# Kernel tuning notes

Hardware: AMD Instinct MI355X
Metric: run time of the kernel (lower is better)

Reference implementation:

```python
import jax, jax.numpy as jnp
import numpy as np

HEADS = 8
DIM_HEAD = 64


def setup_inputs() -> dict:
    key = jax.random.key(0)
    ks = jax.random.split(key, 4)
    B, C, H, W = 1, 256, 64, 64
    inner = HEADS * DIM_HEAD  # 512
    x = jax.random.normal(ks[0], (B, C, H, W), dtype=jnp.float32)
    norm_w = jnp.ones((C,), dtype=jnp.float32)                      # RMSNorm weight (1,C,1,1) flattened
    w_qkv = jax.random.normal(ks[1], (3 * inner, C), dtype=jnp.float32) * 0.02  # 1x1 conv, no bias
    w_out = jax.random.normal(ks[2], (C, inner), dtype=jnp.float32) * 0.02      # 1x1 conv
    b_out = jax.random.normal(ks[3], (C,), dtype=jnp.float32) * 0.02
    return {"x": x, "norm_w": norm_w, "w_qkv": w_qkv, "w_out": w_out, "b_out": b_out}


def reference(x, norm_w, w_qkv, w_out, b_out):
    B, C, H, W = x.shape
    N = H * W
    # RMSNorm: F.normalize over channel dim (L2, eps clamp) * weight * sqrt(C)
    l2 = jnp.sqrt(jnp.sum(x * x, axis=1, keepdims=True))
    xn = x / jnp.maximum(l2, 1e-12) * norm_w[None, :, None, None] * (C ** 0.5)
    # 1x1 conv QKV = channel matmul
    qkv = jnp.einsum('oc,bchw->bohw', w_qkv, xn)  # [B, 3*inner, H, W]
    q, k, v = jnp.split(qkv, 3, axis=1)

    def split_heads(t):
        # 'b (h d) x y -> b h (x y) d'
        return t.reshape(B, HEADS, DIM_HEAD, N).transpose(0, 1, 3, 2)

    q, k, v = map(split_heads, (q, k, v))
    scale = DIM_HEAD ** -0.5
    scores = jnp.einsum('bhnd,bhmd->bhnm', q, k) * scale  # [B,H,N,N]
    attn = jax.nn.softmax(scores, axis=-1)
    out = jnp.einsum('bhnm,bhmd->bhnd', attn, v)
    # 'b h (x y) d -> b (h d) x y'
    out = out.transpose(0, 1, 3, 2).reshape(B, HEADS * DIM_HEAD, H, W)
    # output 1x1 conv + residual (note: residual is the NORMALIZED x, per source)
    return jnp.einsum('ci,bihw->bchw', w_out, out) + b_out[None, :, None, None] + xn
```

## Files before the change

kernel.cpp:

```cpp
#include <hip/hip_runtime.h>


#define NPIX 4096
#define CIN 256
#define INNER 512
#define NHEAD 8
#define DH 64

typedef _Float16 f16;
typedef __attribute__((ext_vector_type(8))) _Float16 f16x8;
typedef __attribute__((ext_vector_type(4))) float f32x4;

static __device__ __forceinline__ f32x4 mfma_f16(f16x8 a, f16x8 b, f32x4 c) {
  return __builtin_amdgcn_mfma_f32_16x16x32_f16(a, b, c, 0, 0, 0);
}

static __device__ __forceinline__ unsigned pk2(float lo, float hi) {
  return __builtin_bit_cast(unsigned, __builtin_amdgcn_cvt_pkrtz(lo, hi));
}

__global__ __launch_bounds__(256) void k_cvt(const float* __restrict__ a,
                                             f16* __restrict__ b, int n) {
  int i = blockIdx.x * 256 + threadIdx.x;
  if (i < n) b[i] = (f16)a[i];
}

__global__ __launch_bounds__(256) void k_rmsnorm(const float* __restrict__ x,
                                                 const float* __restrict__ w,
                                                 float* __restrict__ xn,
                                                 f16* __restrict__ xnT) {
  const int pi = threadIdx.x & 15, cs = threadIdx.x >> 4;
  const int p = blockIdx.x * 16 + pi;
  __shared__ float red[16][16];
  float ss = 0.f;
  for (int i = 0; i < 16; ++i) {
    float v = x[(cs * 16 + i) * NPIX + p];
    ss += v * v;
  }
  red[cs][pi] = ss;
  __syncthreads();
  float tot = 0.f;
#pragma unroll
  for (int s = 0; s < 16; ++s) tot += red[s][pi];
  float inv = 16.0f / fmaxf(sqrtf(tot), 1e-12f);
  for (int i = 0; i < 16; ++i) {
    int c = cs * 16 + i;
    float v = x[c * NPIX + p] * inv * w[c];
    xn[c * NPIX + p] = v;
    xnT[p * CIN + c] = (f16)v;
  }
}

__global__ __launch_bounds__(256) void k_qkv(const f16* __restrict__ wqkv,
                                             const f16* __restrict__ xnT,
                                             f16* __restrict__ qT,
                                             f16* __restrict__ kT,
                                             f16* __restrict__ vv) {
  const int lane = threadIdx.x & 63, wave = threadIdx.x >> 6;
  const int l15 = lane & 15, quad = lane >> 4;
  const int obase = blockIdx.y * 64 + (wave >> 1) * 32;
  const int pbase = blockIdx.x * 128 + (wave & 1) * 64;
  const int sect = blockIdx.y >> 3;
  f32x4 acc[8];
#pragma unroll
  for (int i = 0; i < 8; ++i) acc[i] = (f32x4){0.f, 0.f, 0.f, 0.f};
#pragma unroll
  for (int kc = 0; kc < CIN / 32; ++kc) {
    f16x8 af[2], bfr[4];
#pragma unroll
    for (int oc = 0; oc < 2; ++oc)
      af[oc] = *(const f16x8*)(wqkv + (size_t)(obase + oc * 16 + l15) * CIN + kc * 32 + quad * 8);
#pragma unroll
    for (int pc = 0; pc < 4; ++pc)
      bfr[pc] = *(const f16x8*)(xnT + (size_t)(pbase + pc * 16 + l15) * CIN + kc * 32 + quad * 8);
    if (sect < 2) {
#pragma unroll
      for (int pc = 0; pc < 4; ++pc)
#pragma unroll
        for (int oc = 0; oc < 2; ++oc)
          acc[pc * 2 + oc] = mfma_f16(bfr[pc], af[oc], acc[pc * 2 + oc]);
    } else {
#pragma unroll
      for (int oc = 0; oc < 2; ++oc)
#pragma unroll
        for (int pc = 0; pc < 4; ++pc)
          acc[oc * 4 + pc] = mfma_f16(af[oc], bfr[pc], acc[oc * 4 + pc]);
    }
  }
  if (sect < 2) {
    f16* dst = (sect == 0) ? qT : kT;
    const float sc = (sect == 0) ? 0.18033688f : 1.0f;
    const int head = blockIdx.y & 7;
    const int dd = (wave >> 1) * 32;
#pragma unroll
    for (int pc = 0; pc < 4; ++pc)
#pragma unroll
      for (int oc = 0; oc < 2; ++oc)
#pragma unroll
        for (int r = 0; r < 4; ++r) {
          int p = pbase + pc * 16 + quad * 4 + r;
          dst[((size_t)(head << 12) + p) * DH + dd + oc * 16 + l15] =
              (f16)(acc[pc * 2 + oc][r] * sc);
        }
  } else {
#pragma unroll
    for (int oc = 0; oc < 2; ++oc)
#pragma unroll
      for (int r = 0; r < 4; ++r) {
        int o = obase + oc * 16 + quad * 4 + r - 2 * INNER;
#pragma unroll
        for (int pc = 0; pc < 4; ++pc)
          vv[(size_t)o * NPIX + pbase + pc * 16 + l15] = (f16)acc[oc * 4 + pc][r];
      }
  }
}

__global__ __launch_bounds__(256, 2) void k_attn(const f16* __restrict__ qT,
                                                 const f16* __restrict__ kT,
                                                 const f16* __restrict__ vv,
                                                 f16* __restrict__ Ows) {
  const int head = blockIdx.y;
  const int tid = threadIdx.x;
  const int wave = tid >> 6, lane = tid & 63;
  const int l15 = lane & 15, quad = lane >> 4;
  const int qb = blockIdx.x * 64;

  __shared__ float Om[4][4][64][17];
  __shared__ float Ll[4][4][16];

  f16x8 qf[4][2];
#pragma unroll
  for (int qt = 0; qt < 4; ++qt)
#pragma unroll
    for (int kc = 0; kc < 2; ++kc)
      qf[qt][kc] = *(const f16x8*)(qT + ((size_t)(head << 12) + qb + qt * 16 + l15) * DH + kc * 32 + quad * 8);

  f32x4 o[4][4], ol[4];
#pragma unroll
  for (int qt = 0; qt < 4; ++qt) {
#pragma unroll
    for (int c = 0; c < 4; ++c) o[qt][c] = (f32x4){0.f, 0.f, 0.f, 0.f};
    ol[qt] = (f32x4){0.f, 0.f, 0.f, 0.f};
  }

  const f16* kbase = kT + (size_t)(head << 12) * DH;
  const f16* vbase = vv + (size_t)(head * DH) * NPIX;
  const int kb0 = wave * (NPIX / 4);
  const int srcA = ((quad & 1) << 5) + l15;
  const int srcB = srcA + 16;
  const bool hiQuad = quad >= 2;
  const f16x8 onesv = {1.f16, 1.f16, 1.f16, 1.f16, 1.f16, 1.f16, 1.f16, 1.f16};

  f16x8 kf[2][2], kfn[2][2];
#pragma unroll
  for (int nc = 0; nc < 2; ++nc)
#pragma unroll
    for (int kc = 0; kc < 2; ++kc)
      kf[nc][kc] = *(const f16x8*)(kbase + (size_t)(kb0 + nc * 16 + l15) * DH + kc * 32 + quad * 8);

  for (int it = 0; it < 32; ++it) {
    const int kb = kb0 + it * 32;
    f16x8 vf[4];
#pragma unroll
    for (int c = 0; c < 4; ++c)
      vf[c] = *(const f16x8*)(vbase + (size_t)(c * 16 + l15) * NPIX + kb + quad * 8);
    const int kbn = kb0 + ((it + 1) & 31) * 32;
#pragma unroll
    for (int nc = 0; nc < 2; ++nc)
#pragma unroll
      for (int kc = 0; kc < 2; ++kc)
        kfn[nc][kc] = *(const f16x8*)(kbase + (size_t)(kbn + nc * 16 + l15) * DH + kc * 32 + quad * 8);

    f32x4 s[4][2];
#pragma unroll
    for (int qt = 0; qt < 4; ++qt)
#pragma unroll
      for (int nc = 0; nc < 2; ++nc) {
        s[qt][nc] = mfma_f16(kf[nc][0], qf[qt][0], (f32x4){0.f, 0.f, 0.f, 0.f});
        s[qt][nc] = mfma_f16(kf[nc][1], qf[qt][1], s[qt][nc]);
      }

#pragma unroll
    for (int qt = 0; qt < 4; ++qt) {
      float p0[4], p1[4];
#pragma unroll
      for (int r = 0; r < 4; ++r) {
        p0[r] = __builtin_amdgcn_exp2f(s[qt][0][r]);
        p1[r] = __builtin_amdgcn_exp2f(s[qt][1][r]);
      }
      unsigned A0 = pk2(p0[0], p0[1]), B0 = pk2(p0[2], p0[3]);
      unsigned A1 = pk2(p1[0], p1[1]), B1 = pk2(p1[2], p1[3]);
      unsigned As = hiQuad ? A1 : A0;
      unsigned Bs = hiQuad ? B1 : B0;
      union { f16x8 v; unsigned u[4]; } pf;
      pf.u[0] = (unsigned)__shfl((int)As, srcA);
      pf.u[1] = (unsigned)__shfl((int)Bs, srcA);
      pf.u[2] = (unsigned)__shfl((int)As, srcB);
      pf.u[3] = (unsigned)__shfl((int)Bs, srcB);
#pragma unroll
      for (int c = 0; c < 4; ++c) o[qt][c] = mfma_f16(vf[c], pf.v, o[qt][c]);
      ol[qt] = mfma_f16(onesv, pf.v, ol[qt]);
    }

#pragma unroll
    for (int nc = 0; nc < 2; ++nc)
#pragma unroll
      for (int kc = 0; kc < 2; ++kc) kf[nc][kc] = kfn[nc][kc];
  }

#pragma unroll
  for (int qt = 0; qt < 4; ++qt) {
    if (quad == 0) Ll[wave][qt][l15] = ol[qt][0];
#pragma unroll
    for (int c = 0; c < 4; ++c)
#pragma unroll
      for (int r = 0; r < 4; ++r)
        Om[wave][qt][c * 16 + quad * 4 + r][l15] = o[qt][c][r];
  }
  __syncthreads();

  const int d = tid & 63;
  const int qg = tid >> 6;
#pragma unroll
  for (int qt = 0; qt < 4; ++qt)
#pragma unroll
    for (int i = 0; i < 4; ++i) {
      int q = qg * 4 + i;
      float O = Om[0][qt][d][q] + Om[1][qt][d][q] + Om[2][qt][d][q] + Om[3][qt][d][q];
      float L = Ll[0][qt][q] + Ll[1][qt][q] + Ll[2][qt][q] + Ll[3][qt][q];
      Ows[((size_t)(head << 12) + qb + qt * 16 + q) * DH + d] = (f16)(O / L);
    }
}

__global__ __launch_bounds__(256) void k_oproj(const f16* __restrict__ wout,
                                               const f16* __restrict__ Ows,
                                               const float* __restrict__ bout,
                                               const float* __restrict__ xn,
                                               float* __restrict__ out) {
  const int lane = threadIdx.x & 63, wave = threadIdx.x >> 6;
  const int l15 = lane & 15, quad = lane >> 4;
  const int mbase = blockIdx.y * 32 + (wave >> 1) * 16;
  const int pbase = blockIdx.x * 64 + (wave & 1) * 32;
  f32x4 acc[2];
  acc[0] = (f32x4){0.f, 0.f, 0.f, 0.f};
  acc[1] = (f32x4){0.f, 0.f, 0.f, 0.f};
#pragma unroll
  for (int kc = 0; kc < INNER / 32; ++kc) {
    f16x8 af = *(const f16x8*)(wout + (size_t)(mbase + l15) * INNER + kc * 32 + quad * 8);
    int i0 = kc * 32 + quad * 8;
    int head = i0 >> 6, d0 = i0 & 63;
#pragma unroll
    for (int pc = 0; pc < 2; ++pc) {
      f16x8 bfr = *(const f16x8*)(Ows + ((size_t)(head << 12) + pbase + pc * 16 + l15) * DH + d0);
      acc[pc] = mfma_f16(af, bfr, acc[pc]);
    }
  }
#pragma unroll
  for (int pc = 0; pc < 2; ++pc)
#pragma unroll
    for (int r = 0; r < 4; ++r) {
      int c = mbase + quad * 4 + r, p = pbase + pc * 16 + l15;
      out[c * NPIX + p] = acc[pc][r] + bout[c] + xn[c * NPIX + p];
    }
}

extern "C" void kernel_launch(void* const* d_in, const int* in_sizes, int n_in,
                              void* d_out, int out_size, void* d_ws, size_t ws_size,
                              hipStream_t stream) {
  (void)in_sizes; (void)n_in; (void)out_size; (void)ws_size;
  const float* x      = (const float*)d_in[0];
  const float* norm_w = (const float*)d_in[1];
  const float* w_qkv  = (const float*)d_in[2];
  const float* w_out  = (const float*)d_in[3];
  const float* b_out  = (const float*)d_in[4];
  float* out = (float*)d_out;

  char* ws = (char*)d_ws;
  float* xn    = (float*)(ws);
  f16* xnT     = (f16*)(ws + (4u << 20));
  f16* qT      = (f16*)(ws + (6u << 20));
  f16* kT      = (f16*)(ws + (10u << 20));
  f16* vv      = (f16*)(ws + (14u << 20));
  f16* Ows     = (f16*)(ws + (18u << 20));
  f16* wqkv_h  = (f16*)(ws + (22u << 20));
  f16* wout_h  = (f16*)(ws + (23u << 20));

  hipLaunchKernelGGL(k_cvt, dim3((3 * INNER * CIN + 255) / 256), dim3(256), 0, stream,
                     w_qkv, wqkv_h, 3 * INNER * CIN);
  hipLaunchKernelGGL(k_cvt, dim3((CIN * INNER + 255) / 256), dim3(256), 0, stream,
                     w_out, wout_h, CIN * INNER);
  hipLaunchKernelGGL(k_rmsnorm, dim3(NPIX / 16), dim3(256), 0, stream, x, norm_w, xn, xnT);
  hipLaunchKernelGGL(k_qkv, dim3(NPIX / 128, 1536 / 64), dim3(256), 0, stream,
                     wqkv_h, xnT, qT, kT, vv);
  hipLaunchKernelGGL(k_attn, dim3(NPIX / 64, NHEAD), dim3(256), 0, stream,
                     qT, kT, vv, Ows);
  hipLaunchKernelGGL(k_oproj, dim3(NPIX / 64, CIN / 32), dim3(256), 0, stream,
                     wout_h, Ows, b_out, xn, out);
}
```

Before: 168.4 us.

## Pack attention partials to fp16 in LDS, raise occupancy, fuse weight conversions

The two fp32-to-fp16 weight conversion kernels are merged into one launch that converts two elements per thread. The attention kernel stores per-wave partial outputs in shared memory as packed fp16 pairs instead of fp32, roughly halving LDS usage, and raises the occupancy hint from 2 to 4 blocks. The grid is flattened with the head in the low bits so neighbouring blocks work on different heads. The final reduction writes packed fp16 pairs and multiplies by a reciprocal instead of dividing. Rounding the partial sums to fp16 before the cross-wave reduction slightly reduces precision, and the higher occupancy target may cause register spills.

```diff
diff --git a/kernel.cpp b/kernel.cpp
--- a/kernel.cpp
+++ b/kernel.cpp
@@ -19,10 +19,28 @@
   return __builtin_bit_cast(unsigned, __builtin_amdgcn_cvt_pkrtz(lo, hi));
 }
 
-__global__ __launch_bounds__(256) void k_cvt(const float* __restrict__ a,
-                                             f16* __restrict__ b, int n) {
-  int i = blockIdx.x * 256 + threadIdx.x;
-  if (i < n) b[i] = (f16)a[i];
+static __device__ __forceinline__ float unpk_lo(unsigned u) {
+  return (float)__builtin_bit_cast(f16, (unsigned short)(u & 0xffffu));
+}
+static __device__ __forceinline__ float unpk_hi(unsigned u) {
+  return (float)__builtin_bit_cast(f16, (unsigned short)(u >> 16));
+}
+
+__global__ __launch_bounds__(256) void k_cvt2(const float* __restrict__ a,
+                                              f16* __restrict__ b, int na,
+                                              const float* __restrict__ c,
+                                              f16* __restrict__ d, int nc) {
+  int i = (blockIdx.x * 256 + threadIdx.x) * 2;
+  if (i < na) {
+    float2 v = *(const float2*)(a + i);
+    ((unsigned*)b)[i >> 1] = pk2(v.x, v.y);
+  } else {
+    int j = i - na;
+    if (j < nc) {
+      float2 v = *(const float2*)(c + j);
+      ((unsigned*)d)[j >> 1] = pk2(v.x, v.y);
+    }
+  }
 }
 
 __global__ __launch_bounds__(256) void k_rmsnorm(const float* __restrict__ x,
@@ -115,17 +133,17 @@
   }
 }
 
-__global__ __launch_bounds__(256, 2) void k_attn(const f16* __restrict__ qT,
+__global__ __launch_bounds__(256, 4) void k_attn(const f16* __restrict__ qT,
                                                  const f16* __restrict__ kT,
                                                  const f16* __restrict__ vv,
                                                  f16* __restrict__ Ows) {
-  const int head = blockIdx.y;
+  const int head = blockIdx.x & 7;
+  const int qb = (blockIdx.x >> 3) * 64;
   const int tid = threadIdx.x;
   const int wave = tid >> 6, lane = tid & 63;
   const int l15 = lane & 15, quad = lane >> 4;
-  const int qb = blockIdx.x * 64;
-
-  __shared__ float Om[4][4][64][17];
+
+  __shared__ unsigned Omp[4][4][16][33];
   __shared__ float Ll[4][4][16];
 
   f16x8 qf[4][2];
@@ -212,23 +230,32 @@
   for (int qt = 0; qt < 4; ++qt) {
     if (quad == 0) Ll[wave][qt][l15] = ol[qt][0];
 #pragma unroll
-    for (int c = 0; c < 4; ++c)
-#pragma unroll
-      for (int r = 0; r < 4; ++r)
-        Om[wave][qt][c * 16 + quad * 4 + r][l15] = o[qt][c][r];
+    for (int c = 0; c < 4; ++c) {
+      Omp[wave][qt][l15][c * 8 + quad * 2] = pk2(o[qt][c][0], o[qt][c][1]);
+      Omp[wave][qt][l15][c * 8 + quad * 2 + 1] = pk2(o[qt][c][2], o[qt][c][3]);
+    }
   }
   __syncthreads();
 
-  const int d = tid & 63;
-  const int qg = tid >> 6;
+  const int dp = tid & 31;
+  const int q0 = tid >> 5;
+  unsigned* OwsU = (unsigned*)Ows;
 #pragma unroll
   for (int qt = 0; qt < 4; ++qt)
 #pragma unroll
-    for (int i = 0; i < 4; ++i) {
-      int q = qg * 4 + i;
-      float O = Om[0][qt][d][q] + Om[1][qt][d][q] + Om[2][qt][d][q] + Om[3][qt][d][q];
-      float L = Ll[0][qt][q] + Ll[1][qt][q] + Ll[2][qt][q] + Ll[3][qt][q];
-      Ows[((size_t)(head << 12) + qb + qt * 16 + q) * DH + d] = (f16)(O / L);
+    for (int h = 0; h < 2; ++h) {
+      int q = q0 + h * 8;
+      float a = 0.f, b = 0.f, L = 0.f;
+#pragma unroll
+      for (int w = 0; w < 4; ++w) {
+        unsigned u = Omp[w][qt][q][dp];
+        a += unpk_lo(u);
+        b += unpk_hi(u);
+        L += Ll[w][qt][q];
+      }
+      float rL = 1.0f / L;
+      OwsU[((size_t)(head << 12) + qb + qt * 16 + q) * (DH / 2) + dp] =
+          pk2(a * rL, b * rL);
     }
 }
 
@@ -285,15 +312,13 @@
   f16* wqkv_h  = (f16*)(ws + (22u << 20));
   f16* wout_h  = (f16*)(ws + (23u << 20));
 
-  hipLaunchKernelGGL(k_cvt, dim3((3 * INNER * CIN + 255) / 256), dim3(256), 0, stream,
-                     w_qkv, wqkv_h, 3 * INNER * CIN);
-  hipLaunchKernelGGL(k_cvt, dim3((CIN * INNER + 255) / 256), dim3(256), 0, stream,
-                     w_out, wout_h, CIN * INNER);
+  const int na = 3 * INNER * CIN, nc = CIN * INNER;
+  hipLaunchKernelGGL(k_cvt2, dim3((na + nc) / 512), dim3(256), 0, stream,
+                     w_qkv, wqkv_h, na, w_out, wout_h, nc);
   hipLaunchKernelGGL(k_rmsnorm, dim3(NPIX / 16), dim3(256), 0, stream, x, norm_w, xn, xnT);
   hipLaunchKernelGGL(k_qkv, dim3(NPIX / 128, 1536 / 64), dim3(256), 0, stream,
                      wqkv_h, xnT, qT, kT, vv);
-  hipLaunchKernelGGL(k_attn, dim3(NPIX / 64, NHEAD), dim3(256), 0, stream,
-                     qT, kT, vv, Ows);
+  hipLaunchKernelGGL(k_attn, dim3(512), dim3(256), 0, stream, qT, kT, vv, Ows);
   hipLaunchKernelGGL(k_oproj, dim3(NPIX / 64, CIN / 32), dim3(256), 0, stream,
                      wout_h, Ows, b_out, xn, out);
 }
```

Measured after the change: 280.4 us. +66.5%, slower.
